# Optimization experiments

Measured on AMD Instinct MI355X. Metric: run time of the kernel, lower is better.

Reference implementation:

```python
import jax, jax.numpy as jnp
import numpy as np

HIDDEN = 2048
NUM_HEADS = 32
NUM_KV_HEADS = 4
HEAD_DIM = 128
EPS = 1e-6
ROPE_THETA = 10000.0
Q_SIZE = NUM_HEADS * HEAD_DIM      # 4096
KV_SIZE = NUM_KV_HEADS * HEAD_DIM  # 512


def setup_inputs() -> dict:
    key = jax.random.key(0)
    k1, k2, k3, k4, k5 = jax.random.split(key, 5)
    T = 2048
    hidden_states = jax.random.normal(k1, (T, HIDDEN), dtype=jnp.float32)
    positions = jnp.arange(T, dtype=jnp.int64)
    # qkv_proj weight: [q_size + 2*kv_size, hidden] (torch Linear convention)
    w_qkv = jax.random.normal(k2, (Q_SIZE + 2 * KV_SIZE, HIDDEN), dtype=jnp.float32) * (HIDDEN ** -0.5)
    # o_proj weight: [hidden, num_heads*head_dim]
    w_o = jax.random.normal(k3, (HIDDEN, Q_SIZE), dtype=jnp.float32) * (Q_SIZE ** -0.5)
    q_norm_w = jnp.ones((HEAD_DIM,), dtype=jnp.float32) + 0.1 * jax.random.normal(k4, (HEAD_DIM,), dtype=jnp.float32)
    k_norm_w = jnp.ones((HEAD_DIM,), dtype=jnp.float32) + 0.1 * jax.random.normal(k5, (HEAD_DIM,), dtype=jnp.float32)
    return {"positions": positions, "hidden_states": hidden_states,
            "w_qkv": w_qkv, "w_o": w_o, "q_norm_w": q_norm_w, "k_norm_w": k_norm_w}


def _rms_norm(x, w):
    # x: [..., head_dim]; normalize over last dim
    var = jnp.mean(jnp.square(x), axis=-1, keepdims=True)
    return x * jax.lax.rsqrt(var + EPS) * w


def _rope(positions, x):
    # neox-style rotary over full head_dim. x: [T, H, D]
    half = HEAD_DIM // 2
    inv_freq = 1.0 / (ROPE_THETA ** (jnp.arange(0, half, dtype=jnp.float32) / half))
    freqs = positions.astype(jnp.float32)[:, None] * inv_freq[None, :]  # [T, half]
    cos = jnp.cos(freqs)[:, None, :]  # [T, 1, half]
    sin = jnp.sin(freqs)[:, None, :]
    x1, x2 = x[..., :half], x[..., half:]
    return jnp.concatenate([x1 * cos - x2 * sin, x2 * cos + x1 * sin], axis=-1)


def reference(positions, hidden_states, w_qkv, w_o, q_norm_w, k_norm_w):
    T = hidden_states.shape[0]
    qkv = hidden_states @ w_qkv.T  # [T, q_size+2*kv_size]
    q, k, v = jnp.split(qkv, [Q_SIZE, Q_SIZE + KV_SIZE], axis=-1)
    q = _rms_norm(q.reshape(T, NUM_HEADS, HEAD_DIM), q_norm_w)
    k = _rms_norm(k.reshape(T, NUM_KV_HEADS, HEAD_DIM), k_norm_w)
    v = v.reshape(T, NUM_KV_HEADS, HEAD_DIM)
    q = _rope(positions, q)
    k = _rope(positions, k)
    # GQA: expand kv heads to query heads
    rep = NUM_HEADS // NUM_KV_HEADS
    k = jnp.repeat(k, rep, axis=1)  # [T, H, D]
    v = jnp.repeat(v, rep, axis=1)
    scale = HEAD_DIM ** -0.5
    scores = jnp.einsum('qhd,khd->hqk', q, k) * scale  # [H, T, T]
    causal = jnp.tril(jnp.ones((T, T), dtype=bool))
    scores = jnp.where(causal[None, :, :], scores, jnp.float32(-1e30))
    probs = jax.nn.softmax(scores, axis=-1)
    attn = jnp.einsum('hqk,khd->qhd', probs, v).reshape(T, Q_SIZE)
    return attn @ w_o.T  # [T, hidden]
```

## Files before the change

kernel.cpp:

```cpp
#include <hip/hip_runtime.h>

#define T_TOK   2048
#define HID     2048
#define NHEADS  32
#define NKV     4
#define HD      128
#define QSZ     4096
#define KVSZ    512
#define QKVW    5120

typedef unsigned short u16;
typedef __bf16 bf16x8 __attribute__((ext_vector_type(8)));
typedef float  f32x4  __attribute__((ext_vector_type(4)));

__device__ __forceinline__ u16 f2bf(float f) {
  unsigned int u = __float_as_uint(f);
  u += 0x7fffu + ((u >> 16) & 1u);
  return (u16)(u >> 16);
}

__device__ __forceinline__ void gl2lds16(const void* g, void* l) {
  __builtin_amdgcn_global_load_lds(
      (const __attribute__((address_space(1))) unsigned int*)g,
      (__attribute__((address_space(3))) unsigned int*)l, 16, 0, 0);
}

__global__ void cvt3_f32_bf16(const float* __restrict__ in0, u16* __restrict__ o0, int n0,
                              const float* __restrict__ in1, u16* __restrict__ o1, int n1,
                              const float* __restrict__ in2, u16* __restrict__ o2, int n2) {
  int i = blockIdx.x * blockDim.x + threadIdx.x;
  const float* in; u16* out;
  if (i < n0)            { in = in0; out = o0; }
  else if (i < n0 + n1)  { in = in1; out = o1; i -= n0; }
  else if (i < n0+n1+n2) { in = in2; out = o2; i -= n0 + n1; }
  else return;
  float4 v = ((const float4*)in)[i];
  ushort4 o;
  o.x = f2bf(v.x); o.y = f2bf(v.y); o.z = f2bf(v.z); o.w = f2bf(v.w);
  ((ushort4*)out)[i] = o;
}

template<int BM>
__launch_bounds__(256, 2)
__global__ void gemm_nt(const u16* __restrict__ A, const u16* __restrict__ B,
                        float* __restrict__ C, int M, int N, int K) {
  constexpr int MI = BM / 32;
  __shared__ __align__(16) u16 As[BM * 32];
  __shared__ __align__(16) u16 Bs[128 * 32];
  const int tid  = threadIdx.x;
  const int wave = tid >> 6, lane = tid & 63;
  const int l15  = lane & 15, quad = lane >> 4;
  const int wr   = wave >> 1, wc = wave & 1;

  const u16* Ab = A + (size_t)blockIdx.y * BM * K;
  const u16* Bb = B + (size_t)blockIdx.x * 128 * K;

  f32x4 acc[MI][4];
#pragma unroll
  for (int i = 0; i < MI; i++)
#pragma unroll
    for (int j = 0; j < 4; j++) acc[i][j] = (f32x4){0.f, 0.f, 0.f, 0.f};

  constexpr int ACH = BM * 32 / 8;
  for (int k0 = 0; k0 < K; k0 += 32) {
#pragma unroll
    for (int s = 0; s < (ACH + 512) / 256; s++) {
      int c = tid + s * 256;
      if (c < ACH) {
        int row = c >> 2, co = (c & 3) * 8;
        gl2lds16(Ab + (size_t)row * K + k0 + co, &As[c * 8]);
      } else {
        int c2 = c - ACH;
        int row = c2 >> 2, co = (c2 & 3) * 8;
        gl2lds16(Bb + (size_t)row * K + k0 + co, &Bs[c2 * 8]);
      }
    }
    __syncthreads();
    bf16x8 af[MI], bf[4];
#pragma unroll
    for (int i = 0; i < MI; i++) af[i] = *(const bf16x8*)&As[(wr * (BM / 2) + i * 16 + l15) * 32 + quad * 8];
#pragma unroll
    for (int j = 0; j < 4; j++) bf[j] = *(const bf16x8*)&Bs[(wc * 64 + j * 16 + l15) * 32 + quad * 8];
#pragma unroll
    for (int i = 0; i < MI; i++)
#pragma unroll
      for (int j = 0; j < 4; j++)
        acc[i][j] = __builtin_amdgcn_mfma_f32_16x16x32_bf16(af[i], bf[j], acc[i][j], 0, 0, 0);
    __syncthreads();
  }

  float* Cb = C + (size_t)blockIdx.y * BM * N + (size_t)blockIdx.x * 128;
#pragma unroll
  for (int i = 0; i < MI; i++) {
    int rbase = wr * (BM / 2) + i * 16 + quad * 4;
#pragma unroll
    for (int j = 0; j < 4; j++) {
      int col = wc * 64 + j * 16 + l15;
#pragma unroll
      for (int r = 0; r < 4; r++) Cb[(size_t)(rbase + r) * N + col] = acc[i][j][r];
    }
  }
}

__global__ void norm_rope(const float* __restrict__ qkv, const int* __restrict__ pos,
                          const float* __restrict__ qw, const float* __restrict__ kw,
                          u16* __restrict__ qB, u16* __restrict__ kB, u16* __restrict__ vB) {
  const int t = blockIdx.x;
  const int wave = threadIdx.x >> 6, l = threadIdx.x & 63;
  const float* row = qkv + (size_t)t * QKVW;

  const float p = (float)pos[t];
  const float fr = p * exp2f(-(float)l * 0.20762050593046014f);
  float sn, cs;
  sincosf(fr, &sn, &cs);

  for (int slot = wave; slot < 40; slot += 4) {
    if (slot < 36) {
      const int   base = (slot < 32) ? slot * 128 : 4096 + (slot - 32) * 128;
      const float* w   = (slot < 32) ? qw : kw;
      float x1 = row[base + l], x2 = row[base + 64 + l];
      float ss = x1 * x1 + x2 * x2;
#pragma unroll
      for (int off = 32; off; off >>= 1) ss += __shfl_xor(ss, off);
      float rs = rsqrtf(ss * (1.f / 128.f) + 1e-6f);
      float n1 = x1 * rs * w[l], n2 = x2 * rs * w[64 + l];
      float o1 = n1 * cs - n2 * sn;
      float o2 = n2 * cs + n1 * sn;
      if (slot < 32) {
        o1 *= 0.08838834764831845f;
        o2 *= 0.08838834764831845f;
        qB[(size_t)t * QSZ + slot * 128 + l]      = f2bf(o1);
        qB[(size_t)t * QSZ + slot * 128 + 64 + l] = f2bf(o2);
      } else {
        kB[(size_t)t * KVSZ + (slot - 32) * 128 + l]      = f2bf(o1);
        kB[(size_t)t * KVSZ + (slot - 32) * 128 + 64 + l] = f2bf(o2);
      }
    } else {
      int vh = slot - 36;
      float x1 = row[4608 + vh * 128 + l];
      float x2 = row[4608 + vh * 128 + 64 + l];
      vB[(size_t)t * KVSZ + vh * 128 + l]      = f2bf(x1);
      vB[(size_t)t * KVSZ + vh * 128 + 64 + l] = f2bf(x2);
    }
  }
}

__global__ void transpose_v(const u16* __restrict__ vB, u16* __restrict__ vT) {
  const int vh = blockIdx.y, tb = blockIdx.x;
  const int d0 = threadIdx.x >> 4;
  const int tc = (threadIdx.x & 15) * 8;
#pragma unroll
  for (int s = 0; s < 8; s++) {
    int dd = d0 + s * 16;
    uint4 v; u16* pv = (u16*)&v;
#pragma unroll
    for (int j = 0; j < 8; j++)
      pv[j] = vB[(size_t)(tb * 128 + tc + j) * KVSZ + vh * 128 + dd];
    *(uint4*)&vT[((size_t)vh * 128 + dd) * T_TOK + tb * 128 + tc] = v;
  }
}

__launch_bounds__(512, 4)
__global__ void attn_fa(const u16* __restrict__ qB, const u16* __restrict__ kB,
                        const u16* __restrict__ vT, u16* __restrict__ oB) {
  const int qb  = (blockIdx.y < 16) ? (15 - (int)blockIdx.x) : (int)blockIdx.x;
  const int h   = blockIdx.y;
  const int kvh = h >> 3;
  __shared__ __align__(16) u16 Kb[2][64 * 16 * 8];
  __shared__ __align__(16) u16 Vb[2][128 * 8 * 8];
  __shared__ __align__(16) u16 Pb[128 * 8 * 8];

  const int tid  = threadIdx.x;
  const int wave = tid >> 6, lane = tid & 63;
  const int l15  = lane & 15, quad = lane >> 4;

  auto stage = [&](int kt, int buf) {
#pragma unroll
    for (int s = 0; s < 2; s++) {
      int c = tid + s * 512;
      int r = c >> 4;
      gl2lds16(kB + (size_t)(kt * 64 + r) * KVSZ + kvh * 128 + ((c & 15) ^ (r & 15)) * 8,
               &Kb[buf][c * 8]);
    }
#pragma unroll
    for (int s = 0; s < 2; s++) {
      int c = tid + s * 512;
      int rv = c >> 3;
      gl2lds16(vT + ((size_t)kvh * 128 + rv) * T_TOK + kt * 64 + ((c & 7) ^ (rv & 7)) * 8,
               &Vb[buf][c * 8]);
    }
  };

  bf16x8 qf[4];
#pragma unroll
  for (int ds = 0; ds < 4; ds++)
    qf[ds] = *(const bf16x8*)(qB + (size_t)(qb * 128 + wave * 16 + l15) * QSZ
                                 + h * 128 + ds * 32 + quad * 8);

  f32x4 o[8];
#pragma unroll
  for (int ni = 0; ni < 8; ni++) o[ni] = (f32x4){0.f, 0.f, 0.f, 0.f};
  float mrow[4], lrow[4];
#pragma unroll
  for (int r = 0; r < 4; r++) { mrow[r] = -3.0e38f; lrow[r] = 0.f; }

  const int nt = 2 * qb + 2;

  stage(0, 0);

  for (int kt = 0; kt < nt; kt++) {
    const int cur = kt & 1;
    __syncthreads();
    if (kt + 1 < nt) stage(kt + 1, cur ^ 1);

    f32x4 sc[4];
#pragma unroll
    for (int ni = 0; ni < 4; ni++) sc[ni] = (f32x4){0.f, 0.f, 0.f, 0.f};
    __builtin_amdgcn_s_setprio(1);
#pragma unroll
    for (int ds = 0; ds < 4; ds++) {
#pragma unroll
      for (int ni = 0; ni < 4; ni++) {
        bf16x8 kf = *(const bf16x8*)&Kb[cur][((ni * 16 + l15) * 16 + ((ds * 4 + quad) ^ l15)) * 8];
        sc[ni] = __builtin_amdgcn_mfma_f32_16x16x32_bf16(qf[ds], kf, sc[ni], 0, 0, 0);
      }
    }
    __builtin_amdgcn_s_setprio(0);

    if (kt >= 2 * qb) {
#pragma unroll
      for (int ni = 0; ni < 4; ni++)
#pragma unroll
        for (int r = 0; r < 4; r++) {
          int key = kt * 64 + ni * 16 + l15;
          int rw  = qb * 128 + wave * 16 + quad * 4 + r;
          if (key > rw) sc[ni][r] = -1.0e30f;
        }
    }

#pragma unroll
    for (int r = 0; r < 4; r++) {
      float mx = sc[0][r];
#pragma unroll
      for (int ni = 1; ni < 4; ni++) mx = fmaxf(mx, sc[ni][r]);
#pragma unroll
      for (int off = 1; off < 16; off <<= 1) mx = fmaxf(mx, __shfl_xor(mx, off));
      if (!__all(mx <= mrow[r] + 8.f)) {
        float mn = fmaxf(mrow[r], mx);
        float al = __expf(mrow[r] - mn);
        mrow[r]  = mn;
        lrow[r] *= al;
#pragma unroll
        for (int ni = 0; ni < 8; ni++) o[ni][r] *= al;
      }
      float rs = 0.f;
#pragma unroll
      for (int ni = 0; ni < 4; ni++) {
        float pv = __expf(sc[ni][r] - mrow[r]);
        sc[ni][r] = pv;
        rs += pv;
      }
#pragma unroll
      for (int off = 1; off < 16; off <<= 1) rs += __shfl_xor(rs, off);
      lrow[r] += rs;
    }

#pragma unroll
    for (int ni = 0; ni < 4; ni++)
#pragma unroll
      for (int r = 0; r < 4; r++) {
        int row = wave * 16 + quad * 4 + r;
        Pb[(row * 8 + ((ni * 2 + (l15 >> 3)) ^ (row & 7))) * 8 + (l15 & 7)] =
            f2bf(sc[ni][r]);
      }

    __builtin_amdgcn_s_setprio(1);
#pragma unroll
    for (int ks = 0; ks < 2; ks++) {
      bf16x8 pf = *(const bf16x8*)&Pb[((wave * 16 + l15) * 8 + ((ks * 4 + quad) ^ (l15 & 7))) * 8];
#pragma unroll
      for (int ni = 0; ni < 8; ni++) {
        bf16x8 vf = *(const bf16x8*)&Vb[cur][((ni * 16 + l15) * 8 + ((ks * 4 + quad) ^ (l15 & 7))) * 8];
        o[ni] = __builtin_amdgcn_mfma_f32_16x16x32_bf16(pf, vf, o[ni], 0, 0, 0);
      }
    }
    __builtin_amdgcn_s_setprio(0);
  }

#pragma unroll
  for (int ni = 0; ni < 8; ni++)
#pragma unroll
    for (int r = 0; r < 4; r++) {
      int t = qb * 128 + wave * 16 + quad * 4 + r;
      float val = o[ni][r] / lrow[r];
      oB[(size_t)t * QSZ + h * 128 + ni * 16 + l15] = f2bf(val);
    }
}

extern "C" void kernel_launch(void* const* d_in, const int* in_sizes, int n_in,
                              void* d_out, int out_size, void* d_ws, size_t ws_size,
                              hipStream_t stream) {
  const int*   positions = (const int*)d_in[0];
  const float* hidden    = (const float*)d_in[1];
  const float* w_qkv     = (const float*)d_in[2];
  const float* w_o       = (const float*)d_in[3];
  const float* qw        = (const float*)d_in[4];
  const float* kw        = (const float*)d_in[5];
  float* out = (float*)d_out;
  char*  ws  = (char*)d_ws;

  u16* hiddenB = (u16*)ws;
  u16* wqkvB   = hiddenB + (size_t)HID * HID;
  u16* woB     = wqkvB + (size_t)QKVW * HID;
  size_t off1  = ((size_t)HID * HID + (size_t)QKVW * HID + (size_t)HID * QSZ) * 2;
  float* qkvF  = (float*)(ws + off1);
  u16*   attnB = (u16*)(ws + off1);
  size_t off2  = off1 + (size_t)T_TOK * QKVW * 4;
  u16* qBuf = (u16*)(ws + off2);
  size_t off3  = off2 + (size_t)T_TOK * QSZ * 2;
  u16* kBuf = (u16*)(ws + off3);
  size_t off4  = off3 + (size_t)T_TOK * KVSZ * 2;
  u16* vTb  = (u16*)(ws + off4);
  size_t off5  = off4 + (size_t)T_TOK * KVSZ * 2;
  u16* vBuf = (u16*)(ws + off5);

  const int n0 = HID * HID / 4, n1 = QKVW * HID / 4, n2 = HID * QSZ / 4;
  cvt3_f32_bf16<<<(n0 + n1 + n2 + 255) / 256, 256, 0, stream>>>(
      hidden, hiddenB, n0, w_qkv, wqkvB, n1, w_o, woB, n2);

  gemm_nt<128><<<dim3(QKVW / 128, T_TOK / 128), 256, 0, stream>>>(hiddenB, wqkvB, qkvF, T_TOK, QKVW, HID);

  norm_rope<<<T_TOK, 256, 0, stream>>>(qkvF, positions, qw, kw, qBuf, kBuf, vBuf);

  transpose_v<<<dim3(T_TOK / 128, NKV), 256, 0, stream>>>(vBuf, vTb);

  attn_fa<<<dim3(T_TOK / 128, NHEADS), 512, 0, stream>>>(qBuf, kBuf, vTb, attnB);

  gemm_nt<64><<<dim3(HID / 128, T_TOK / 64), 256, 0, stream>>>(attnB, woB, out, T_TOK, HID, QSZ);
}
```

Before: 366.5 us.

## Swizzle GEMM block order, use exp2 softmax with DPP row reductions

The GEMM remaps workgroup ids with an XCD-aware swizzle so neighbouring tiles share L2 on the same die. The log2(e) factor is folded into the Q scale so softmax can use exp2f directly. The 16-lane max and sum reductions now use DPP row_ror moves instead of ds_swizzle shuffles. The epilogue computes one reciprocal per row instead of dividing every element. Together these target cache locality and ALU and LDS overhead in the attention inner loop. The swizzle assumes the block count is divisible by 8, and the rotate DPP reductions rely on the lane layout to give correct row results.

```diff
diff --git a/kernel.cpp b/kernel.cpp
--- a/kernel.cpp
+++ b/kernel.cpp
@@ -23,6 +23,17 @@
   __builtin_amdgcn_global_load_lds(
       (const __attribute__((address_space(1))) unsigned int*)g,
       (__attribute__((address_space(3))) unsigned int*)l, 16, 0, 0);
+}
+
+template<int N>
+__device__ __forceinline__ float rotmax(float x) {
+  int t = __builtin_amdgcn_mov_dpp(__float_as_int(x), 0x120 | N, 0xf, 0xf, true);
+  return fmaxf(x, __int_as_float(t));
+}
+template<int N>
+__device__ __forceinline__ float rotadd(float x) {
+  int t = __builtin_amdgcn_mov_dpp(__float_as_int(x), 0x120 | N, 0xf, 0xf, true);
+  return x + __int_as_float(t);
 }
 
 __global__ void cvt3_f32_bf16(const float* __restrict__ in0, u16* __restrict__ o0, int n0,
@@ -52,8 +63,14 @@
   const int l15  = lane & 15, quad = lane >> 4;
   const int wr   = wave >> 1, wc = wave & 1;
 
-  const u16* Ab = A + (size_t)blockIdx.y * BM * K;
-  const u16* Bb = B + (size_t)blockIdx.x * 128 * K;
+  const int nwg = gridDim.x * gridDim.y;
+  int lid = blockIdx.y * gridDim.x + blockIdx.x;
+  lid = (lid & 7) * (nwg >> 3) + (lid >> 3);
+  const int bx = lid % gridDim.x;
+  const int by = lid / gridDim.x;
+
+  const u16* Ab = A + (size_t)by * BM * K;
+  const u16* Bb = B + (size_t)bx * 128 * K;
 
   f32x4 acc[MI][4];
 #pragma unroll
@@ -89,7 +106,7 @@
     __syncthreads();
   }
 
-  float* Cb = C + (size_t)blockIdx.y * BM * N + (size_t)blockIdx.x * 128;
+  float* Cb = C + (size_t)by * BM * N + (size_t)bx * 128;
 #pragma unroll
   for (int i = 0; i < MI; i++) {
     int rbase = wr * (BM / 2) + i * 16 + quad * 4;
@@ -109,6 +126,8 @@
   const int wave = threadIdx.x >> 6, l = threadIdx.x & 63;
   const float* row = qkv + (size_t)t * QKVW;
 
+  constexpr float QSC = 0.08838834764831845f * 1.4426950408889634f;
+
   const float p = (float)pos[t];
   const float fr = p * exp2f(-(float)l * 0.20762050593046014f);
   float sn, cs;
@@ -127,8 +146,8 @@
       float o1 = n1 * cs - n2 * sn;
       float o2 = n2 * cs + n1 * sn;
       if (slot < 32) {
-        o1 *= 0.08838834764831845f;
-        o2 *= 0.08838834764831845f;
+        o1 *= QSC;
+        o2 *= QSC;
         qB[(size_t)t * QSZ + slot * 128 + l]      = f2bf(o1);
         qB[(size_t)t * QSZ + slot * 128 + 64 + l] = f2bf(o2);
       } else {
@@ -240,14 +259,11 @@
 
 #pragma unroll
     for (int r = 0; r < 4; r++) {
-      float mx = sc[0][r];
-#pragma unroll
-      for (int ni = 1; ni < 4; ni++) mx = fmaxf(mx, sc[ni][r]);
-#pragma unroll
-      for (int off = 1; off < 16; off <<= 1) mx = fmaxf(mx, __shfl_xor(mx, off));
+      float mx = fmaxf(fmaxf(sc[0][r], sc[1][r]), fmaxf(sc[2][r], sc[3][r]));
+      mx = rotmax<1>(mx); mx = rotmax<2>(mx); mx = rotmax<4>(mx); mx = rotmax<8>(mx);
       if (!__all(mx <= mrow[r] + 8.f)) {
         float mn = fmaxf(mrow[r], mx);
-        float al = __expf(mrow[r] - mn);
+        float al = exp2f(mrow[r] - mn);
         mrow[r]  = mn;
         lrow[r] *= al;
 #pragma unroll
@@ -256,12 +272,11 @@
       float rs = 0.f;
 #pragma unroll
       for (int ni = 0; ni < 4; ni++) {
-        float pv = __expf(sc[ni][r] - mrow[r]);
+        float pv = exp2f(sc[ni][r] - mrow[r]);
         sc[ni][r] = pv;
         rs += pv;
       }
-#pragma unroll
-      for (int off = 1; off < 16; off <<= 1) rs += __shfl_xor(rs, off);
+      rs = rotadd<1>(rs); rs = rotadd<2>(rs); rs = rotadd<4>(rs); rs = rotadd<8>(rs);
       lrow[r] += rs;
     }
 
@@ -288,13 +303,13 @@
   }
 
 #pragma unroll
-  for (int ni = 0; ni < 8; ni++)
-#pragma unroll
-    for (int r = 0; r < 4; r++) {
-      int t = qb * 128 + wave * 16 + quad * 4 + r;
-      float val = o[ni][r] / lrow[r];
-      oB[(size_t)t * QSZ + h * 128 + ni * 16 + l15] = f2bf(val);
-    }
+  for (int r = 0; r < 4; r++) {
+    float rinv = 1.0f / lrow[r];
+    int t = qb * 128 + wave * 16 + quad * 4 + r;
+#pragma unroll
+    for (int ni = 0; ni < 8; ni++)
+      oB[(size_t)t * QSZ + h * 128 + ni * 16 + l15] = f2bf(o[ni][r] * rinv);
+  }
 }
 
 extern "C" void kernel_launch(void* const* d_in, const int* in_sizes, int n_in,
```

Result: no change. 359.9 us (-1.8%).
